# Performance work log

Measured on AMD Instinct MI355X. Metric: run time of the kernel, lower is better.

The kernel has to match this reference:

```python
import jax, jax.numpy as jnp
import numpy as np

SEQ = 2048
D = 2048          # d_model
H = 16            # n_heads
DH = D // H       # dim_per_head = 128 (= pe_rotary_dims, full-head RoPE)
DFF = 4 * D
BACKGROUND_LEN = 1024
STYLE_VECS_LEN = 64


def setup_inputs() -> dict:
    key = jax.random.key(0)
    ks = jax.random.split(key, 12)
    s = 0.02
    f32 = jnp.float32
    return {
        "x": jax.random.normal(ks[0], (SEQ, D), f32),
        "attn_bias": jnp.zeros((SEQ, SEQ), f32),
        "ln_scale": jnp.ones((D,), f32),
        "ln_offset": jnp.zeros((D,), f32),
        "Wq": (jax.random.normal(ks[1], (D, D), f32) * s),
        "Wk": (jax.random.normal(ks[2], (D, D), f32) * s),
        "Wv": (jax.random.normal(ks[3], (D, D), f32) * s),
        "Wo": (jax.random.normal(ks[4], (D, D), f32) * s),
        "W1": (jax.random.normal(ks[5], (D, DFF), f32) * s),
        "b1": jnp.zeros((DFF,), f32),
        "W2": (jax.random.normal(ks[6], (DFF, D), f32) * s),
        "b2": jnp.zeros((D,), f32),
    }


def _layernorm(x, scale, offset):
    mean = jnp.mean(x, axis=-1, keepdims=True)
    var = jnp.var(x, axis=-1, keepdims=True)
    return scale * jax.lax.rsqrt(var + 1e-5) * (x - mean) + offset


def _rotate_every_two(x):
    # x: (T, H, d) -> interleaved (-x2, x1)
    x1 = x[:, :, ::2]
    x2 = x[:, :, 1::2]
    return jnp.stack((-x2, x1), axis=-1).reshape(x.shape)


def _apply_rope(q, k):
    rd = q.shape[-1]
    inv_freq = 1.0 / 10000 ** (np.arange(0, rd, 2) / rd)  # (rd/2,)
    pos = jnp.arange(k.shape[0])
    sinusoid = pos[:, None] * inv_freq[None, :]           # (T, rd/2)
    # repeat 'b n -> b (n j)', j=2  ==  elementwise repeat along last axis
    sin = jnp.repeat(jnp.sin(sinusoid), 2, axis=-1)[:, None, :]  # (T,1,rd)
    cos = jnp.repeat(jnp.cos(sinusoid), 2, axis=-1)[:, None, :]
    q = q * cos + _rotate_every_two(q) * sin
    k = k * cos + _rotate_every_two(k) * sin
    return q, k


def _causal_bottleneck_bias():
    mask = np.tril(np.ones((SEQ, SEQ), np.float32))
    # DO_CAUSAL_BOTTLENECK: tokens after background+style cannot see background
    mask[BACKGROUND_LEN + STYLE_VECS_LEN:, :BACKGROUND_LEN] = 0.0
    return jnp.asarray(-1e10 * (1.0 - mask))


def reference(x, attn_bias, ln_scale, ln_offset, Wq, Wk, Wv, Wo, W1, b1, W2, b2):
    # f_psum / g_psum are identities with cores_per_replica == 1
    xn = _layernorm(x, ln_scale, ln_offset)                      # (T, D)

    q = (xn @ Wq).reshape(SEQ, H, DH)
    k = (xn @ Wk).reshape(SEQ, H, DH)
    v = (xn @ Wv).reshape(SEQ, H, DH)

    q, k = _apply_rope(q, k)  # pe_rotary_dims == dim_per_head: rotate whole head

    logits = jnp.einsum('thd,Thd->htT', q, k) / np.sqrt(DH).astype(x.dtype)
    bias = _causal_bottleneck_bias() + attn_bias                 # (T, T)
    logits = logits + bias[None, :, :]
    weights = jax.nn.softmax(logits, axis=-1)                    # (H, T, T)

    attn_vec = jnp.einsum('htT,Thd->thd', weights, v).reshape(SEQ, D)
    attn_out = attn_vec @ Wo                                     # (T, D)

    ff = jax.nn.gelu(xn @ W1 + b1) @ W2 + b2                     # (T, D)
    return attn_out + ff
```

## Files before the change

### kernel.cpp

```cpp
#include <hip/hip_runtime.h>

#define SEQ 2048
#define DMODEL 2048
#define NH 16
#define DH 128
#define DFF 8192

typedef __bf16 bf16x8 __attribute__((ext_vector_type(8)));
typedef float f32x4 __attribute__((ext_vector_type(4)));
typedef int i32x4 __attribute__((ext_vector_type(4)));

__device__ __forceinline__ float b2f(unsigned short u) {
    union { float f; unsigned int i; } v; v.i = ((unsigned int)u) << 16; return v.f;
}
__device__ __forceinline__ unsigned short f2b(float f) {
    union { float f; unsigned int i; } v; v.f = f;
    unsigned int i = v.i;
    i += 0x7fffu + ((i >> 16) & 1u);
    return (unsigned short)(i >> 16);
}
__device__ __forceinline__ bf16x8 ldfrag(const unsigned short* p) {
    return *(const bf16x8*)p;
}
__device__ __forceinline__ void async_ld16(const void* g, void* l) {
    __builtin_amdgcn_global_load_lds(
        (const __attribute__((address_space(1))) unsigned int*)g,
        (__attribute__((address_space(3))) unsigned int*)l, 16, 0, 0);
}
__device__ __forceinline__ float loadef(const void* p, long i, int isf) {
    return isf ? ((const float*)p)[i] : b2f(((const unsigned short*)p)[i]);
}
__device__ __forceinline__ void load8f(const void* p, long i, int isf, float* v) {
    if (isf) {
        i32x4 r0 = *(const i32x4*)((const float*)p + i);
        i32x4 r1 = *(const i32x4*)((const float*)p + i + 4);
        const float* f0 = (const float*)&r0;
        const float* f1 = (const float*)&r1;
#pragma unroll
        for (int j = 0; j < 4; j++) { v[j] = f0[j]; v[4 + j] = f1[j]; }
    } else {
        i32x4 raw = *(const i32x4*)((const unsigned short*)p + i);
        const unsigned short* u = (const unsigned short*)&raw;
#pragma unroll
        for (int j = 0; j < 8; j++) v[j] = b2f(u[j]);
    }
}

__global__ __launch_bounds__(256) void detect_kernel(const unsigned short* __restrict__ x,
                                                     int* __restrict__ flag)
{
    const int tid = threadIdx.x;
    int bad = 0;
#pragma unroll
    for (int i = 0; i < 16; i++) {
        unsigned short u = x[tid * 16 + i];
        int e = (u >> 7) & 0xFF;
        if (e >= 0x90) bad = 1;
    }
    unsigned long long b = __ballot(bad);
    __shared__ int r[4];
    if ((tid & 63) == 0) r[tid >> 6] = (b != 0ull);
    __syncthreads();
    if (tid == 0) *flag = (r[0] | r[1] | r[2] | r[3]) ? 1 : 0;
}

__global__ __launch_bounds__(256) void ln_kernel(
    const void* __restrict__ x,
    const void* __restrict__ sc,
    const void* __restrict__ of,
    unsigned short* __restrict__ xn,
    const int* __restrict__ fl)
{
    const int isf = *fl;
    const int row = blockIdx.x, tid = threadIdx.x;
    float v[8]; float s = 0.f, sq = 0.f;
    load8f(x, (long)row * DMODEL + tid * 8, isf, v);
#pragma unroll
    for (int i = 0; i < 8; i++) { s += v[i]; sq += v[i] * v[i]; }
#pragma unroll
    for (int off = 1; off < 64; off <<= 1) { s += __shfl_xor(s, off); sq += __shfl_xor(sq, off); }
    __shared__ float red[8];
    const int w = tid >> 6, l = tid & 63;
    if (l == 0) { red[w * 2] = s; red[w * 2 + 1] = sq; }
    __syncthreads();
    s  = red[0] + red[2] + red[4] + red[6];
    sq = red[1] + red[3] + red[5] + red[7];
    const float mean = s * (1.0f / DMODEL);
    const float var  = sq * (1.0f / DMODEL) - mean * mean;
    const float rsig = rsqrtf(var + 1e-5f);
    __align__(16) unsigned short o[8];
#pragma unroll
    for (int i = 0; i < 8; i++) {
        int c = tid * 8 + i;
        o[i] = f2b(loadef(sc, c, isf) * (v[i] - mean) * rsig + loadef(of, c, isf));
    }
    *(i32x4*)(xn + (long)row * DMODEL + tid * 8) = *(const i32x4*)o;
}

__global__ __launch_bounds__(1024) void transpose_w(
    const void* __restrict__ in0, const void* __restrict__ in1,
    const void* __restrict__ in2, const void* __restrict__ in3,
    unsigned short* __restrict__ out, int R, int C,
    const int* __restrict__ fl)
{
    const int isf = *fl;
    const int z = blockIdx.z;
    const void* in = (z == 0) ? in0 : (z == 1) ? in1 : (z == 2) ? in2 : in3;
    unsigned short* dst = out + (long)z * R * C;
    __shared__ unsigned int tile[32][33];
    const int tx = threadIdx.x, ty = threadIdx.y;
    const int c0 = blockIdx.x * 32, r0 = blockIdx.y * 64;
    const float a0 = loadef(in, (long)(r0 + 2 * ty)     * C + c0 + tx, isf);
    const float a1 = loadef(in, (long)(r0 + 2 * ty + 1) * C + c0 + tx, isf);
    tile[ty][tx] = (unsigned)f2b(a0) | ((unsigned)f2b(a1) << 16);
    __syncthreads();
    *(unsigned int*)(dst + (long)(c0 + ty) * R + r0 + 2 * tx) = tile[tx][ty];
}

__global__ __launch_bounds__(256) void rope_kernel(unsigned short* q, unsigned short* k)
{
    const int idx = blockIdx.x * 256 + threadIdx.x;
    const int i = idx & 63;
    const int h = (idx >> 6) & 15;
    const int t = idx >> 10;
    const long base = (long)t * DMODEL + h * DH + 2 * i;
    const float inv = __expf(-(float)i * (9.210340371976184f / 64.0f));
    float sn, cs;
    sincosf((float)t * inv, &sn, &cs);
    {
        float a = b2f(q[base]), b = b2f(q[base + 1]);
        q[base]     = f2b(a * cs - b * sn);
        q[base + 1] = f2b(b * cs + a * sn);
    }
    {
        float a = b2f(k[base]), b = b2f(k[base + 1]);
        k[base]     = f2b(a * cs - b * sn);
        k[base + 1] = f2b(b * cs + a * sn);
    }
}

template<int EPI>
__global__ __launch_bounds__(256) void gemm_bt(
    const unsigned short* __restrict__ A,
    const unsigned short* __restrict__ Bt,
    const void* __restrict__ bias,
    const unsigned short* __restrict__ add,
    void* __restrict__ Cout,
    int M, int N, int K, int Ks,
    const int* __restrict__ fl)
{
    const int isf = fl ? *fl : 0;
    __shared__ __align__(16) unsigned short lA[128 * 64];
    __shared__ __align__(16) unsigned short lB[128 * 64];
    const int tid = threadIdx.x;
    const int l = tid & 63, w = tid >> 6;
    const int quad = l >> 4, lq = l & 15;
    const long bm = (long)blockIdx.y * 128, bn = (long)blockIdx.x * 128;
    const int wm = (w >> 1) * 64, wn = (w & 1) * 64;
    const int kofs = (EPI == 5) ? blockIdx.z * Ks : 0;

    const int r8 = l >> 3;
    const int csw = ((l & 7) ^ r8) * 8;
    const unsigned short* Ag = A  + (bm + w * 32 + r8) * (long)K + kofs + csw;
    const unsigned short* Bg = Bt + (bn + w * 32 + r8) * (long)K + kofs + csw;
    unsigned short* lAd = lA + w * 2048 + l * 8;
    unsigned short* lBd = lB + w * 2048 + l * 8;
    const long K8 = 8 * (long)K;

    f32x4 acc[4][4] = {};

    for (int k0 = 0; k0 < Ks; k0 += 64) {
#pragma unroll
        for (int q = 0; q < 4; q++) {
            async_ld16(Ag + k0 + q * K8, lAd + q * 512);
            async_ld16(Bg + k0 + q * K8, lBd + q * 512);
        }
        __syncthreads();
#pragma unroll
        for (int hk = 0; hk < 2; hk++) {
            bf16x8 af[4], bfv[4];
#pragma unroll
            for (int i = 0; i < 4; i++) {
                const int row = wm + i * 16 + lq;
                af[i] = ldfrag(lA + row * 64 + ((hk * 4 + quad) ^ (lq & 7)) * 8);
            }
#pragma unroll
            for (int j = 0; j < 4; j++) {
                const int row = wn + j * 16 + lq;
                bfv[j] = ldfrag(lB + row * 64 + ((hk * 4 + quad) ^ (lq & 7)) * 8);
            }
#pragma unroll
            for (int i = 0; i < 4; i++)
#pragma unroll
                for (int j = 0; j < 4; j++)
                    acc[i][j] = __builtin_amdgcn_mfma_f32_16x16x32_bf16(af[i], bfv[j], acc[i][j], 0, 0, 0);
        }
        __syncthreads();
    }

#pragma unroll
    for (int i = 0; i < 4; i++)
#pragma unroll
        for (int j = 0; j < 4; j++)
#pragma unroll
            for (int r = 0; r < 4; r++) {
                const long t = bm + wm + i * 16 + quad * 4 + r;
                const long n = bn + wn + j * 16 + lq;
                float v = acc[i][j][r];
                if constexpr (EPI == 5) {
                    ((float*)Cout)[(long)blockIdx.z * M * N + t * N + n] = v;
                } else if constexpr (EPI == 4) {
                    unsigned short* base = (unsigned short*)Cout;
                    if (n < 4096)
                        base[(n >> 11) * (long)(SEQ * DMODEL) + t * DMODEL + (n & 2047)] = f2b(v);
                    else {
                        const long np = n - 4096;
                        base[2L * SEQ * DMODEL + (np >> 7) * (long)(DH * SEQ) + (np & 127) * (long)SEQ + t] = f2b(v);
                    }
                } else if constexpr (EPI == 3) {
                    v += loadef(bias, n, isf) + b2f(add[t * (long)N + n]);
                    if (isf) ((float*)Cout)[t * (long)N + n] = v;
                    else     ((unsigned short*)Cout)[t * (long)N + n] = f2b(v);
                } else {
                    if constexpr (EPI == 2) {
                        v += loadef(bias, n, isf);
                        const float u = 0.7978845608028654f * (v + 0.044715f * v * v * v);
                        v = v * (1.0f - __builtin_amdgcn_rcpf(1.0f + __expf(2.0f * u)));
                    }
                    ((unsigned short*)Cout)[t * (long)N + n] = f2b(v);
                }
            }
}

__global__ __launch_bounds__(256) void reduce_out(
    const float* __restrict__ P, int nsplit,
    const unsigned short* __restrict__ aout,
    const void* __restrict__ b2,
    void* __restrict__ out,
    const int* __restrict__ fl)
{
    const int isf = *fl;
    const long i = ((long)blockIdx.x * 256 + threadIdx.x) * 4;
    f32x4 s = *(const f32x4*)(P + i);
    for (int z = 1; z < nsplit; z++) s += *(const f32x4*)(P + (long)z * SEQ * DMODEL + i);
    const unsigned short* a4 = aout + i;
    float v[4];
#pragma unroll
    for (int c = 0; c < 4; c++)
        v[c] = s[c] + b2f(a4[c]) + loadef(b2, (i + c) & (DMODEL - 1), isf);
    if (isf) {
        f32x4 o; o[0] = v[0]; o[1] = v[1]; o[2] = v[2]; o[3] = v[3];
        *(f32x4*)((float*)out + i) = o;
    } else {
        __align__(8) unsigned short o[4];
#pragma unroll
        for (int c = 0; c < 4; c++) o[c] = f2b(v[c]);
        *(unsigned long long*)((unsigned short*)out + i) = *(const unsigned long long*)o;
    }
}

__global__ __launch_bounds__(256) void flash_attn(
    const unsigned short* __restrict__ q,
    const unsigned short* __restrict__ k,
    const unsigned short* __restrict__ vT,
    const void* __restrict__ bias,
    unsigned short* __restrict__ outp,
    const int* __restrict__ fl)
{
    const int isf = *fl;
    __shared__ __align__(16) unsigned short lK[64 * 128];
    __shared__ __align__(16) unsigned short lV[128 * 64];
    __shared__ __align__(16) float          lBf[64 * 64];
    __shared__ __align__(16) unsigned short lP[4 * 16 * 72];
    unsigned short* lBh = (unsigned short*)lBf;
    const int tid = threadIdx.x;
    const int l = tid & 63, w = tid >> 6;
    const int quad = l >> 4, lq = l & 15;
    const int qb = blockIdx.x * 64;
    const int h = blockIdx.y;

    bf16x8 aq[4];
#pragma unroll
    for (int c = 0; c < 4; c++)
        aq[c] = ldfrag(q + (long)(qb + 16 * w + lq) * DMODEL + h * DH + 32 * c + quad * 8);

    f32x4 accO[8] = {};
    float m_i[4], l_i[4];
#pragma unroll
    for (int r = 0; r < 4; r++) { m_i[r] = -1e30f; l_i[r] = 0.f; }

    const int Tstart = (qb >= 1088) ? 1024 : 0;
    unsigned short* lPw = lP + w * (16 * 72);
    const int rowmax_w = qb + 16 * w + 15;

    const unsigned short* kh = k + h * DH;
    const unsigned short* vh = vT + (long)h * (DH * SEQ);

    for (int Tt = Tstart; Tt < qb + 64; Tt += 64) {
        __syncthreads();
#pragma unroll
        for (int s = 0; s < 4; s++) {
            const int ci = s * 256 + tid;
            const int rr = ci >> 4, p = ci & 15;
            async_ld16(kh + (long)(Tt + rr) * DMODEL + (p ^ (rr & 15)) * 8,
                       lK + ci * 8);
        }
#pragma unroll
        for (int s = 0; s < 4; s++) {
            const int ci = s * 256 + tid;
            const int dd = ci >> 3, p = ci & 7;
            async_ld16(vh + (long)dd * SEQ + Tt + (p ^ (dd & 7)) * 8,
                       lV + ci * 8);
        }
        if (isf) {
            const float* bsrc = (const float*)bias;
#pragma unroll
            for (int s = 0; s < 4; s++) {
                const int ci = s * 256 + tid;
                const int rr = ci >> 4, cc = ci & 15;
                async_ld16(bsrc + (long)(qb + rr) * SEQ + Tt + cc * 4, lBf + ci * 4);
            }
        } else {
            const unsigned short* bsrc = (const unsigned short*)bias;
#pragma unroll
            for (int s = 0; s < 2; s++) {
                const int ci = s * 256 + tid;
                const int rr = ci >> 3, cc = ci & 7;
                async_ld16(bsrc + (long)(qb + rr) * SEQ + Tt + cc * 8, lBh + ci * 8);
            }
        }
        __syncthreads();
        if (Tt > rowmax_w) continue;

        float sv[4][4];
        float mx[4] = { -1e30f, -1e30f, -1e30f, -1e30f };
#pragma unroll
        for (int j = 0; j < 4; j++) {
            f32x4 accS = {};
#pragma unroll
            for (int c = 0; c < 4; c++) {
                bf16x8 bk = ldfrag(lK + (j * 16 + lq) * 128 + ((4 * c + quad) ^ lq) * 8);
                accS = __builtin_amdgcn_mfma_f32_16x16x32_bf16(aq[c], bk, accS, 0, 0, 0);
            }
            const int Tcol = Tt + j * 16 + lq;
#pragma unroll
            for (int r = 0; r < 4; r++) {
                const int rloc = 16 * w + quad * 4 + r;
                const int trow = qb + rloc;
                float s;
                if (Tcol > trow) s = -1e30f;
                else {
                    const float bv = isf ? lBf[rloc * 64 + j * 16 + lq]
                                         : b2f(lBh[rloc * 64 + j * 16 + lq]);
                    s = accS[r] * 0.08838834764831845f + bv;
                }
                sv[j][r] = s;
                mx[r] = fmaxf(mx[r], s);
            }
        }
#pragma unroll
        for (int r = 0; r < 4; r++) {
            mx[r] = fmaxf(mx[r], __shfl_xor(mx[r], 1));
            mx[r] = fmaxf(mx[r], __shfl_xor(mx[r], 2));
            mx[r] = fmaxf(mx[r], __shfl_xor(mx[r], 4));
            mx[r] = fmaxf(mx[r], __shfl_xor(mx[r], 8));
        }
        float alpha[4];
#pragma unroll
        for (int r = 0; r < 4; r++) {
            const float mn = fmaxf(m_i[r], mx[r]);
            alpha[r] = __expf(m_i[r] - mn);
            m_i[r] = mn;
            float sum = 0.f;
#pragma unroll
            for (int j = 0; j < 4; j++) {
                const float p = __expf(sv[j][r] - mn);
                sv[j][r] = p;
                sum += p;
            }
            sum += __shfl_xor(sum, 1);
            sum += __shfl_xor(sum, 2);
            sum += __shfl_xor(sum, 4);
            sum += __shfl_xor(sum, 8);
            l_i[r] = l_i[r] * alpha[r] + sum;
        }
#pragma unroll
        for (int j = 0; j < 4; j++)
#pragma unroll
            for (int r = 0; r < 4; r++)
                lPw[(quad * 4 + r) * 72 + j * 16 + lq] = f2b(sv[j][r]);
#pragma unroll
        for (int jd = 0; jd < 8; jd++)
#pragma unroll
            for (int r = 0; r < 4; r++)
                accO[jd][r] *= alpha[r];
        const bf16x8 ap0 = ldfrag(lPw + lq * 72 + quad * 8);
        const bf16x8 ap1 = ldfrag(lPw + lq * 72 + 32 + quad * 8);
#pragma unroll
        for (int jd = 0; jd < 8; jd++) {
            bf16x8 bv0 = ldfrag(lV + (jd * 16 + lq) * 64 + (quad ^ (lq & 7)) * 8);
            accO[jd] = __builtin_amdgcn_mfma_f32_16x16x32_bf16(ap0, bv0, accO[jd], 0, 0, 0);
            bf16x8 bv1 = ldfrag(lV + (jd * 16 + lq) * 64 + ((quad + 4) ^ (lq & 7)) * 8);
            accO[jd] = __builtin_amdgcn_mfma_f32_16x16x32_bf16(ap1, bv1, accO[jd], 0, 0, 0);
        }
    }
#pragma unroll
    for (int r = 0; r < 4; r++) {
        const float inv = 1.0f / l_i[r];
        const long trow = qb + 16 * w + quad * 4 + r;
#pragma unroll
        for (int jd = 0; jd < 8; jd++)
            outp[trow * (long)DMODEL + h * DH + jd * 16 + lq] = f2b(accO[jd][r] * inv);
    }
}

extern "C" void kernel_launch(void* const* d_in, const int* in_sizes, int n_in,
                              void* d_out, int out_size, void* d_ws, size_t ws_size,
                              hipStream_t stream)
{
    (void)in_sizes; (void)n_in; (void)out_size;
    const void* x         = d_in[0];
    const void* attn_bias = d_in[1];
    const void* ln_scale  = d_in[2];
    const void* ln_offset = d_in[3];
    const void* Wq = d_in[4];
    const void* Wk = d_in[5];
    const void* Wv = d_in[6];
    const void* Wo = d_in[7];
    const void* W1 = d_in[8];
    const void* b1 = d_in[9];
    const void* W2 = d_in[10];
    const void* b2 = d_in[11];

    char* ws = (char*)d_ws;
    unsigned short* wT   = (unsigned short*)(ws);
    unsigned short* xn   = (unsigned short*)(ws + (32ull << 20));
    unsigned short* qv   = (unsigned short*)(ws + (40ull << 20));
    unsigned short* kv   = (unsigned short*)(ws + (48ull << 20));
    unsigned short* vTb  = (unsigned short*)(ws + (56ull << 20));
    unsigned short* avec = (unsigned short*)(ws + (64ull << 20));
    unsigned short* aout = (unsigned short*)(ws + (72ull << 20));
    unsigned short* hff  = (unsigned short*)(ws + (40ull << 20));
    int* flag            = (int*)(ws + (80ull << 20));
    float* Pf            = (float*)(ws + (81ull << 20));

    int nsplit = 1;
    if (ws_size >= (145ull << 20)) nsplit = 4;
    else if (ws_size >= (113ull << 20)) nsplit = 2;

    const dim3 tb(32, 32);

    detect_kernel<<<1, 256, 0, stream>>>((const unsigned short*)x, flag);

    ln_kernel<<<SEQ, 256, 0, stream>>>(x, ln_scale, ln_offset, xn, flag);

    transpose_w<<<dim3(64, 32, 4), tb, 0, stream>>>(Wq, Wk, Wv, Wo, wT, DMODEL, DMODEL, flag);

    gemm_bt<4><<<dim3(48, 16), 256, 0, stream>>>(xn, wT, nullptr, nullptr, qv,
                                                 SEQ, 3 * DMODEL, DMODEL, DMODEL, flag);

    rope_kernel<<<(SEQ * NH * DH / 2) / 256, 256, 0, stream>>>(qv, kv);

    flash_attn<<<dim3(SEQ / 64, NH), 256, 0, stream>>>(qv, kv, vTb, attn_bias, avec, flag);

    gemm_bt<0><<<dim3(16, 16), 256, 0, stream>>>(avec, wT + 12ull * 1024 * 1024, nullptr, nullptr, aout,
                                                 SEQ, DMODEL, DMODEL, DMODEL, flag);

    transpose_w<<<dim3(DFF / 32, DMODEL / 64), tb, 0, stream>>>(W1, W1, W1, W1, wT, DMODEL, DFF, flag);
    gemm_bt<2><<<dim3(DFF / 128, SEQ / 128), 256, 0, stream>>>(xn, wT, b1, nullptr, hff,
                                                               SEQ, DFF, DMODEL, DMODEL, flag);

    transpose_w<<<dim3(DMODEL / 32, DFF / 64), tb, 0, stream>>>(W2, W2, W2, W2, wT, DFF, DMODEL, flag);
    if (nsplit > 1) {
        gemm_bt<5><<<dim3(16, 16, nsplit), 256, 0, stream>>>(hff, wT, nullptr, nullptr, Pf,
                                                             SEQ, DMODEL, DFF, DFF / nsplit, flag);
        reduce_out<<<(SEQ * DMODEL) / (256 * 4), 256, 0, stream>>>(Pf, nsplit, aout, b2, d_out, flag);
    } else {
        gemm_bt<3><<<dim3(16, 16), 256, 0, stream>>>(hff, wT, b2, aout, d_out,
                                                     SEQ, DMODEL, DFF, DFF, flag);
    }
}
```

Measured before the change: 644.9 us.

## Double-buffer GEMM LDS tiles with K-step 32 to overlap loads and MFMA

Rewrites the main GEMM loop to use two LDS buffers of 128x32 per operand instead of one 128x64 buffer. The next K-slice is prefetched asynchronously into the other buffer while MFMAs run on the current one, with a single barrier per step. The goal is to hide global-to-LDS latency behind compute. In exchange the K-step is halved, so barriers per K and loop overhead double, and the swizzle is redone for 32-wide rows.

```diff
diff --git a/kernel.cpp b/kernel.cpp
--- a/kernel.cpp
+++ b/kernel.cpp
@@ -150,8 +150,8 @@
     const int* __restrict__ fl)
 {
     const int isf = fl ? *fl : 0;
-    __shared__ __align__(16) unsigned short lA[128 * 64];
-    __shared__ __align__(16) unsigned short lB[128 * 64];
+    __shared__ __align__(16) unsigned short lA[2][128 * 32];
+    __shared__ __align__(16) unsigned short lB[2][128 * 32];
     const int tid = threadIdx.x;
     const int l = tid & 63, w = tid >> 6;
     const int quad = l >> 4, lq = l & 15;
@@ -159,42 +159,47 @@
     const int wm = (w >> 1) * 64, wn = (w & 1) * 64;
     const int kofs = (EPI == 5) ? blockIdx.z * Ks : 0;
 
-    const int r8 = l >> 3;
-    const int csw = ((l & 7) ^ r8) * 8;
-    const unsigned short* Ag = A  + (bm + w * 32 + r8) * (long)K + kofs + csw;
-    const unsigned short* Bg = Bt + (bn + w * 32 + r8) * (long)K + kofs + csw;
-    unsigned short* lAd = lA + w * 2048 + l * 8;
-    unsigned short* lBd = lB + w * 2048 + l * 8;
-    const long K8 = 8 * (long)K;
+    const int r16 = l >> 2;
+    const int sel = (l >> 3) & 3;
+    const int csw = ((l & 3) ^ sel) * 8;
+    const unsigned short* Ag0 = A  + (bm + w * 32 + r16) * (long)K + kofs + csw;
+    const unsigned short* Ag1 = Ag0 + 16 * (long)K;
+    const unsigned short* Bg0 = Bt + (bn + w * 32 + r16) * (long)K + kofs + csw;
+    const unsigned short* Bg1 = Bg0 + 16 * (long)K;
+    const int ld0 = (w * 128 + l) * 8;
+    const int ld1 = (w * 128 + 64 + l) * 8;
+    const int selr = (lq >> 1) & 3;
 
     f32x4 acc[4][4] = {};
 
-    for (int k0 = 0; k0 < Ks; k0 += 64) {
-#pragma unroll
-        for (int q = 0; q < 4; q++) {
-            async_ld16(Ag + k0 + q * K8, lAd + q * 512);
-            async_ld16(Bg + k0 + q * K8, lBd + q * 512);
-        }
-        __syncthreads();
-#pragma unroll
-        for (int hk = 0; hk < 2; hk++) {
-            bf16x8 af[4], bfv[4];
-#pragma unroll
-            for (int i = 0; i < 4; i++) {
-                const int row = wm + i * 16 + lq;
-                af[i] = ldfrag(lA + row * 64 + ((hk * 4 + quad) ^ (lq & 7)) * 8);
-            }
-#pragma unroll
-            for (int j = 0; j < 4; j++) {
-                const int row = wn + j * 16 + lq;
-                bfv[j] = ldfrag(lB + row * 64 + ((hk * 4 + quad) ^ (lq & 7)) * 8);
-            }
-#pragma unroll
-            for (int i = 0; i < 4; i++)
-#pragma unroll
-                for (int j = 0; j < 4; j++)
-                    acc[i][j] = __builtin_amdgcn_mfma_f32_16x16x32_bf16(af[i], bfv[j], acc[i][j], 0, 0, 0);
-        }
+    const int nsteps = Ks >> 5;
+    async_ld16(Ag0, &lA[0][ld0]);
+    async_ld16(Ag1, &lA[0][ld1]);
+    async_ld16(Bg0, &lB[0][ld0]);
+    async_ld16(Bg1, &lB[0][ld1]);
+    __syncthreads();
+
+    for (int s = 0; s < nsteps; s++) {
+        const int b = s & 1;
+        if (s + 1 < nsteps) {
+            const int kk = (s + 1) << 5;
+            async_ld16(Ag0 + kk, &lA[1 - b][ld0]);
+            async_ld16(Ag1 + kk, &lA[1 - b][ld1]);
+            async_ld16(Bg0 + kk, &lB[1 - b][ld0]);
+            async_ld16(Bg1 + kk, &lB[1 - b][ld1]);
+        }
+        bf16x8 af[4], bfv[4];
+#pragma unroll
+        for (int i = 0; i < 4; i++)
+            af[i]  = ldfrag(&lA[b][(wm + i * 16 + lq) * 32 + ((quad ^ selr) * 8)]);
+#pragma unroll
+        for (int j = 0; j < 4; j++)
+            bfv[j] = ldfrag(&lB[b][(wn + j * 16 + lq) * 32 + ((quad ^ selr) * 8)]);
+#pragma unroll
+        for (int i = 0; i < 4; i++)
+#pragma unroll
+            for (int j = 0; j < 4; j++)
+                acc[i][j] = __builtin_amdgcn_mfma_f32_16x16x32_bf16(af[i], bfv[j], acc[i][j], 0, 0, 0);
         __syncthreads();
     }
 
```

After: 649.8 us. Within noise of the previous version (+0.8%).
